# Kernel optimization log

Measured on AMD Instinct MI355X. Metric: run time of the kernel, lower is better.

Reference implementation:

```python
import jax, jax.numpy as jnp
import numpy as np

D_MODEL = 32   # channels arg = Mamba d_model
D_INNER = 32   # expand=1
D_STATE = 8
DT_RANK = 2    # ceil(32/16)
D_CONV = 4


def layer_norm(h, g, b, eps=1e-5):
    m = jnp.mean(h, axis=-1, keepdims=True)
    v = jnp.var(h, axis=-1, keepdims=True)
    return (h - m) * jax.lax.rsqrt(v + eps) * g + b


def causal_conv1d(h, w, b):
    # h: [B, d, L]; w: [d, K] depthwise; torch Conv1d(padding=K-1) truncated to first L
    out = jax.lax.conv_general_dilated(h, w[:, None, :], (1,), [(D_CONV - 1, 0)],
                                       dimension_numbers=('NCH', 'OIH', 'NCH'),
                                       feature_group_count=h.shape[1])
    return out + b[None, :, None]


def selective_scan(u, delta, A, Bm, Cm, D):
    # u, delta: [B, d, L]; A: [d, n]; Bm, Cm: [B, n, L]; D: [d]
    dA = jnp.exp(jnp.einsum('bdl,dn->lbdn', delta, A))       # [L, B, d, n]
    dBu = jnp.einsum('bdl,bnl,bdl->lbdn', delta, Bm, u)      # [L, B, d, n]
    Cseq = jnp.transpose(Cm, (2, 0, 1))                      # [L, B, n]
    h0 = jnp.zeros((u.shape[0], A.shape[0], A.shape[1]), u.dtype)

    def step(h, inp):
        dA_t, dBu_t, C_t = inp
        h = dA_t * h + dBu_t
        return h, jnp.einsum('bdn,bn->bd', h, C_t)

    _, ys = jax.lax.scan(step, h0, (dA, dBu, Cseq))          # ys: [L, B, d]
    return jnp.transpose(ys, (1, 2, 0)) + D[None, :, None] * u


def mamba_direction(xz, conv_w, conv_b, xproj_w, dtproj_w, dtproj_b, A_log, D):
    xh, z = jnp.split(xz, 2, axis=1)                         # each [B, d_inner, L]
    xh = jax.nn.silu(causal_conv1d(xh, conv_w, conv_b))
    x_dbl = jnp.einsum('bdl,kd->bkl', xh, xproj_w)           # [B, dt_rank+2n, L]
    dt, Bm, Cm = jnp.split(x_dbl, [DT_RANK, DT_RANK + D_STATE], axis=1)
    dt = jax.nn.softplus(jnp.einsum('brl,dr->bdl', dt, dtproj_w) + dtproj_b[None, :, None])
    y = selective_scan(xh, dt, -jnp.exp(A_log), Bm, Cm, D)
    return y * jax.nn.silu(z)


def forward(x, lin1_w, lin1_b, ln1_g, ln1_b, in_proj_w,
            conv_w_f, conv_b_f, xproj_w_f, dtproj_w_f, dtproj_b_f, A_log_f, D_f,
            conv_w_r, conv_b_r, xproj_w_r, dtproj_w_r, dtproj_b_r, A_log_r, D_r,
            out_proj_w, mnorm_g, mnorm_b, lin2_w, lin2_b):
    avg = jnp.mean(x, axis=(2, 3))                           # [B, C] adaptive avg pool
    mx = jnp.max(x, axis=(2, 3))                             # [B, C] adaptive max pool
    combined = jnp.stack([avg, mx], axis=-1)                 # [B, C, 2]
    h = combined @ lin1_w.T + lin1_b                         # [B, C, d_model]
    h = layer_norm(h, ln1_g, ln1_b)
    # bidirectional Mamba (bimamba v2) over sequence length L = C
    xz = jnp.einsum('blc,ec->bel', h, in_proj_w)             # [B, 2*d_inner, L]
    out_f = mamba_direction(xz, conv_w_f, conv_b_f, xproj_w_f, dtproj_w_f, dtproj_b_f, A_log_f, D_f)
    out_r = mamba_direction(xz[..., ::-1], conv_w_r, conv_b_r, xproj_w_r, dtproj_w_r, dtproj_b_r, A_log_r, D_r)[..., ::-1]
    out = (out_f + out_r) / 2.0                              # if_devide_out=True
    out = jnp.einsum('bdl,od->blo', out, out_proj_w)         # [B, L, d_model]
    out = layer_norm(out, mnorm_g, mnorm_b)                  # use_norm=True
    att = jax.nn.sigmoid(out @ lin2_w.T + lin2_b)            # [B, L, 1]
    return att[..., None] * 0.25 + 0.875                     # [B, C, 1, 1]


def setup_inputs() -> dict:
    key = jax.random.key(0)
    ks = jax.random.split(key, 12)
    B, C, H, W = 32, 512, 64, 64

    def rn(k, shape, s):
        return jax.random.normal(k, shape, jnp.float32) * s

    A_log = jnp.log(jnp.broadcast_to(jnp.arange(1, D_STATE + 1, dtype=jnp.float32), (D_INNER, D_STATE)))
    return {
        'x': jax.random.normal(ks[0], (B, C, H, W), jnp.float32),
        'lin1_w': rn(ks[1], (D_MODEL, 2), 0.5),
        'lin1_b': jnp.zeros((D_MODEL,), jnp.float32),
        'ln1_g': jnp.ones((D_MODEL,), jnp.float32),
        'ln1_b': jnp.zeros((D_MODEL,), jnp.float32),
        'in_proj_w': rn(ks[2], (2 * D_INNER, D_MODEL), 0.1),
        'conv_w_f': rn(ks[3], (D_INNER, D_CONV), 0.3),
        'conv_b_f': jnp.zeros((D_INNER,), jnp.float32),
        'xproj_w_f': rn(ks[4], (DT_RANK + 2 * D_STATE, D_INNER), 0.1),
        'dtproj_w_f': rn(ks[5], (D_INNER, DT_RANK), 0.5),
        'dtproj_b_f': jnp.full((D_INNER,), -4.6, jnp.float32),
        'A_log_f': A_log,
        'D_f': jnp.ones((D_INNER,), jnp.float32),
        'conv_w_r': rn(ks[6], (D_INNER, D_CONV), 0.3),
        'conv_b_r': jnp.zeros((D_INNER,), jnp.float32),
        'xproj_w_r': rn(ks[7], (DT_RANK + 2 * D_STATE, D_INNER), 0.1),
        'dtproj_w_r': rn(ks[8], (D_INNER, DT_RANK), 0.5),
        'dtproj_b_r': jnp.full((D_INNER,), -4.6, jnp.float32),
        'A_log_r': A_log,
        'D_r': jnp.ones((D_INNER,), jnp.float32),
        'out_proj_w': rn(ks[9], (D_MODEL, D_INNER), 0.1),
        'mnorm_g': jnp.ones((D_MODEL,), jnp.float32),
        'mnorm_b': jnp.zeros((D_MODEL,), jnp.float32),
        'lin2_w': rn(ks[10], (1, D_MODEL), 0.3),
        'lin2_b': jnp.zeros((1,), jnp.float32),
    }


def reference(x, lin1_w, lin1_b, ln1_g, ln1_b, in_proj_w,
              conv_w_f, conv_b_f, xproj_w_f, dtproj_w_f, dtproj_b_f, A_log_f, D_f,
              conv_w_r, conv_b_r, xproj_w_r, dtproj_w_r, dtproj_b_r, A_log_r, D_r,
              out_proj_w, mnorm_g, mnorm_b, lin2_w, lin2_b):
    return forward(x, lin1_w, lin1_b, ln1_g, ln1_b, in_proj_w,
                   conv_w_f, conv_b_f, xproj_w_f, dtproj_w_f, dtproj_b_f, A_log_f, D_f,
                   conv_w_r, conv_b_r, xproj_w_r, dtproj_w_r, dtproj_b_r, A_log_r, D_r,
                   out_proj_w, mnorm_g, mnorm_b, lin2_w, lin2_b)
```

## Files before the change

kernel.cpp:

```cpp
#include <hip/hip_runtime.h>
#include <math.h>

#define BB 32
#define CC 512
#define HW 4096
#define DM 32
#define DI 32
#define DS 8
#define KC 4

#define NCH 16
#define CHL 32

__device__ __forceinline__ float siluf(float x) {
    return x / (1.0f + __expf(-x));
}
__device__ __forceinline__ float softplusf(float x) {
    float ax = fabsf(x);
    return fmaxf(x, 0.0f) + log1pf(__expf(-ax));
}

__global__ __launch_bounds__(256) void poolproj_kernel(
    const float* __restrict__ x,
    const float* __restrict__ lin1_w, const float* __restrict__ lin1_b,
    const float* __restrict__ ln1_g, const float* __restrict__ ln1_b,
    const float* __restrict__ in_proj_w, float* __restrict__ xz)
{
    __shared__ float sWp[64][33];
    int tid = threadIdx.x;
    for (int i = tid; i < 64 * DM; i += 256) sWp[i >> 5][i & 31] = in_proj_w[i];
    __syncthreads();

    int wave = tid >> 6, lane = tid & 63;
    int row = blockIdx.x * 4 + wave;
    const float4* xp = reinterpret_cast<const float4*>(x + (size_t)row * HW);
    float s = 0.f, m = -INFINITY;
#pragma unroll
    for (int k = 0; k < 16; ++k) {
        float4 v = xp[k * 64 + lane];
        s += (v.x + v.y) + (v.z + v.w);
        m = fmaxf(m, fmaxf(fmaxf(v.x, v.y), fmaxf(v.z, v.w)));
    }
#pragma unroll
    for (int off = 1; off < 64; off <<= 1) {
        s += __shfl_xor(s, off);
        m = fmaxf(m, __shfl_xor(m, off));
    }
    float a = s * (1.0f / HW);
    int m_ = lane & 31;
    float h = a * lin1_w[2 * m_] + m * lin1_w[2 * m_ + 1] + lin1_b[m_];
    float sum = h;
#pragma unroll
    for (int mask = 1; mask < 32; mask <<= 1) sum += __shfl_xor(sum, mask);
    float mean = sum * (1.0f / DM);
    float d = h - mean;
    float vs = d * d;
#pragma unroll
    for (int mask = 1; mask < 32; mask <<= 1) vs += __shfl_xor(vs, mask);
    float rs = rsqrtf(vs * (1.0f / DM) + 1e-5f);
    float hn = d * rs * ln1_g[m_] + ln1_b[m_];
    float acc = 0.f;
#pragma unroll
    for (int mm = 0; mm < DM; ++mm)
        acc += __shfl(hn, mm) * sWp[lane][mm];
    xz[((size_t)row << 6) + lane] = acc;
}

__global__ __launch_bounds__(512) void convscan1_kernel(
    const float* __restrict__ xz,
    const float* __restrict__ conv_w_f, const float* __restrict__ conv_b_f,
    const float* __restrict__ xproj_w_f, const float* __restrict__ dtproj_w_f,
    const float* __restrict__ dtproj_b_f,
    const float* __restrict__ conv_w_r, const float* __restrict__ conv_b_r,
    const float* __restrict__ xproj_w_r, const float* __restrict__ dtproj_w_r,
    const float* __restrict__ dtproj_b_r,
    const float* __restrict__ A_log_f, const float* __restrict__ A_log_r,
    float* __restrict__ u_g, float* __restrict__ dt_g,
    float* __restrict__ B_g, float* __restrict__ C_g,
    float* __restrict__ carrA, float* __restrict__ carrH)
{
    int bx = blockIdx.x;
    int b = bx >> 4, t = bx & 15;
    int tid = threadIdx.x;
    int L0 = t * CHL;

    __shared__ float xt[32][41];
    __shared__ float xw_s[2][18][33];
    __shared__ float u_s[2][CHL][33];
    __shared__ float dt_s[2][CHL][33];
    __shared__ float B_s[2][CHL][9];
    __shared__ float C_s[2][CHL][9];
    __shared__ float dtr_s[2][CHL][2];

    for (int idx = tid; idx < 38 * 32; idx += 512) {
        int c = idx >> 5, dd = idx & 31;
        int col = L0 - 3 + c;
        float v = 0.f;
        if (col >= 0 && col < 512)
            v = xz[(((size_t)b * 512 + col) << 6) + dd];
        xt[dd][c] = v;
    }
    for (int idx = tid; idx < 2 * 18 * 32; idx += 512) {
        int dirw = idx >= 576;
        int r2 = idx - dirw * 576;
        const float* xw = dirw ? xproj_w_r : xproj_w_f;
        xw_s[dirw][r2 >> 5][r2 & 31] = xw[r2];
    }
    __syncthreads();

#pragma unroll
    for (int p = 0; p < 4; ++p) {
        int idx = p * 512 + tid;
        int dd = idx & 31, l = (idx >> 5) & 31, dirw = idx >> 10;
        const float* cw2 = dirw ? conv_w_r : conv_w_f;
        const float* cb2 = dirw ? conv_b_r : conv_b_f;
        float acc = cb2[dd];
        if (dirw == 0) {
#pragma unroll
            for (int k = 0; k < KC; ++k) acc += cw2[dd * KC + k] * xt[dd][l + k];
        } else {
#pragma unroll
            for (int jj = 0; jj < KC; ++jj) acc += cw2[dd * KC + 3 - jj] * xt[dd][l + 3 + jj];
        }
        u_s[dirw][l][dd] = siluf(acc);
    }
    __syncthreads();

#pragma unroll
    for (int p = 0; p < 3; ++p) {
        int idx = p * 512 + tid;
        if (idx < 1152) {
            int dirw = idx >= 576;
            int r2 = idx - dirw * 576;
            int o = r2 >> 5, l = r2 & 31;
            float acc = 0.f;
#pragma unroll
            for (int m_ = 0; m_ < 32; ++m_) acc += u_s[dirw][l][m_] * xw_s[dirw][o][m_];
            if (o < 2)       dtr_s[dirw][l][o] = acc;
            else if (o < 10) B_s[dirw][l][o - 2] = acc;
            else             C_s[dirw][l][o - 10] = acc;
        }
    }
    __syncthreads();

#pragma unroll
    for (int p = 0; p < 4; ++p) {
        int idx = p * 512 + tid;
        int dd = idx & 31, l = (idx >> 5) & 31, dirw = idx >> 10;
        const float* dw2 = dirw ? dtproj_w_r : dtproj_w_f;
        const float* db2 = dirw ? dtproj_b_r : dtproj_b_f;
        float v = dtr_s[dirw][l][0] * dw2[dd * 2] + dtr_s[dirw][l][1] * dw2[dd * 2 + 1] + db2[dd];
        dt_s[dirw][l][dd] = softplusf(v);
    }
    __syncthreads();

#pragma unroll
    for (int p = 0; p < 4; ++p) {
        int idx = p * 512 + tid;
        int dd = idx & 31, l = (idx >> 5) & 31, dirw = idx >> 10;
        int sp = dirw ? (511 - (L0 + l)) : (L0 + l);
        size_t g = ((size_t)(b * 2 + dirw) * 512 + sp) * 32 + dd;
        u_g[g]  = u_s[dirw][l][dd];
        dt_g[g] = dt_s[dirw][l][dd];
    }
    {
        int dirw = tid >> 8;
        int r2 = tid & 255;
        int l = r2 >> 3, n = r2 & 7;
        int sp = dirw ? (511 - (L0 + l)) : (L0 + l);
        size_t g = ((size_t)(b * 2 + dirw) * 512 + sp) * 8 + n;
        B_g[g] = B_s[dirw][l][n];
        C_g[g] = C_s[dirw][l][n];
    }

    {
        int dir = tid >> 8;
        int tid2 = tid & 255;
        int dd = tid2 >> 3, nn = tid2 & 7;
        int jc = dir ? (15 - t) : t;
        const float* Alog = dir ? A_log_r : A_log_f;
        float Aa = -__expf(Alog[tid2]);
        float ap = 1.f, h = 0.f;
#pragma unroll 4
        for (int sl = 0; sl < CHL; ++sl) {
            int ll = dir ? (CHL - 1 - sl) : sl;
            float dtv = dt_s[dir][ll][dd];
            float uu  = u_s[dir][ll][dd];
            float bm  = B_s[dir][ll][nn];
            float dA  = __expf(dtv * Aa);
            ap *= dA;
            h = dA * h + dtv * uu * bm;
        }
        size_t cidx = (((size_t)(b * 2 + dir) * NCH + jc) << 8) + tid2;
        carrA[cidx] = ap;
        carrH[cidx] = h;
    }
}

__global__ __launch_bounds__(512) void scan2final_kernel(
    const float* __restrict__ u_g, const float* __restrict__ dt_g,
    const float* __restrict__ B_g, const float* __restrict__ C_g,
    const float* __restrict__ carrA, const float* __restrict__ carrH,
    const float* __restrict__ A_log_f, const float* __restrict__ D_f,
    const float* __restrict__ A_log_r, const float* __restrict__ D_r,
    const float* __restrict__ xz,
    const float* __restrict__ out_proj_w, const float* __restrict__ mnorm_g,
    const float* __restrict__ mnorm_b, const float* __restrict__ lin2_w,
    const float* __restrict__ lin2_b, float* __restrict__ out)
{
    int bx = blockIdx.x;
    int b = bx >> 4, t = bx & 15;
    int tid = threadIdx.x;
    int L0 = t * CHL;

    __shared__ float u_s[2][CHL][33];
    __shared__ float dt_s[2][CHL][33];
    __shared__ float B_s[2][CHL][12];
    __shared__ float C_s[2][CHL][12];
    __shared__ float z_s[CHL][33];
    __shared__ float y_s[2][CHL][33];
    __shared__ float comb_s[CHL][33];
    __shared__ float opw_s[DM][33];

    for (int idx = tid; idx < 2 * CHL * 32; idx += 512) {
        int dirw = idx >> 10;
        int r2 = idx & 1023;
        int sl = r2 >> 5, d = r2 & 31;
        int bd = b * 2 + dirw;
        int tc = dirw ? (15 - t) : t;
        size_t g = ((size_t)bd * 512 + tc * CHL + sl) * 32 + d;
        u_s[dirw][sl][d]  = u_g[g];
        dt_s[dirw][sl][d] = dt_g[g];
    }
    {
        int dirw = tid >> 8;
        int r2 = tid & 255;
        int sl = r2 >> 3, n = r2 & 7;
        int bd = b * 2 + dirw;
        int tc = dirw ? (15 - t) : t;
        size_t g = ((size_t)bd * 512 + tc * CHL + sl) * 8 + n;
        B_s[dirw][sl][n] = B_g[g];
        C_s[dirw][sl][n] = C_g[g];
    }
    for (int idx = tid; idx < CHL * 32; idx += 512) {
        int l = idx >> 5, d = idx & 31;
        z_s[l][d] = xz[(((size_t)b * 512 + L0 + l) << 6) + 32 + d];
        opw_s[idx >> 5][d] = out_proj_w[idx];
    }
    __syncthreads();

    {
        int dir = tid >> 8;
        int r = tid & 255;
        int d = r >> 3, n = r & 7;
        int bd = b * 2 + dir;
        int tt = dir ? (15 - t) : t;
        const float* Alog = dir ? A_log_r : A_log_f;
        const float* Dp   = dir ? D_r : D_f;
        float A  = -__expf(Alog[r]);
        float Dd = Dp[d];

        float h = 0.f;
        for (int g4 = 0; g4 < 4; ++g4) {
            int jbase = g4 * 4;
            if (jbase >= tt) break;
            float av[4], hv[4];
#pragma unroll
            for (int k = 0; k < 4; ++k) {
                int jj = jbase + k;
                int js = (jj < tt) ? jj : 0;
                size_t cb2 = (((size_t)bd * NCH + js) << 8) + r;
                av[k] = carrA[cb2];
                hv[k] = carrH[cb2];
            }
#pragma unroll
            for (int k = 0; k < 4; ++k)
                if (jbase + k < tt) h = av[k] * h + hv[k];
        }

#pragma unroll 4
        for (int sl = 0; sl < CHL; ++sl) {
            float dtv = dt_s[dir][sl][d];
            float uu  = u_s[dir][sl][d];
            float bm  = B_s[dir][sl][n];
            float cm  = C_s[dir][sl][n];
            h = __expf(dtv * A) * h + dtv * uu * bm;
            float py = h * cm;
            py += __shfl_xor(py, 1);
            py += __shfl_xor(py, 2);
            py += __shfl_xor(py, 4);
            if (n == 0) {
                int ll = dir ? (CHL - 1 - sl) : sl;
                y_s[dir][ll][d] = py + Dd * uu;
            }
        }
    }
    __syncthreads();

    for (int idx = tid; idx < CHL * 32; idx += 512) {
        int l = idx >> 5, d = idx & 31;
        comb_s[l][d] = 0.5f * (y_s[0][l][d] + y_s[1][l][d]) * siluf(z_s[l][d]);
    }
    __syncthreads();

    {
        int l = tid >> 4, k = tid & 15;
        float oa = 0.f, ob = 0.f;
#pragma unroll
        for (int d = 0; d < DI; ++d) {
            float c = comb_s[l][d];
            oa += c * opw_s[k][d];
            ob += c * opw_s[k + 16][d];
        }
        float sum = oa + ob;
#pragma unroll
        for (int mask = 1; mask < 16; mask <<= 1) sum += __shfl_xor(sum, mask);
        float mean = sum * (1.0f / DM);
        float da = oa - mean, db2 = ob - mean;
        float vs = da * da + db2 * db2;
#pragma unroll
        for (int mask = 1; mask < 16; mask <<= 1) vs += __shfl_xor(vs, mask);
        float rs = rsqrtf(vs * (1.0f / DM) + 1e-5f);
        float va = da * rs * mnorm_g[k] + mnorm_b[k];
        float vb = db2 * rs * mnorm_g[k + 16] + mnorm_b[k + 16];
        float sv = va * lin2_w[k] + vb * lin2_w[k + 16];
#pragma unroll
        for (int mask = 1; mask < 16; mask <<= 1) sv += __shfl_xor(sv, mask);
        if (k == 0) {
            float att = 1.0f / (1.0f + __expf(-(sv + lin2_b[0])));
            out[(size_t)b * 512 + L0 + l] = 0.25f * att + 0.875f;
        }
    }
}

extern "C" void kernel_launch(void* const* d_in, const int* in_sizes, int n_in,
                              void* d_out, int out_size, void* d_ws, size_t ws_size,
                              hipStream_t stream)
{
    const float* x         = (const float*)d_in[0];
    const float* lin1_w    = (const float*)d_in[1];
    const float* lin1_b    = (const float*)d_in[2];
    const float* ln1_g     = (const float*)d_in[3];
    const float* ln1_b     = (const float*)d_in[4];
    const float* in_proj_w = (const float*)d_in[5];
    const float* conv_w_f  = (const float*)d_in[6];
    const float* conv_b_f  = (const float*)d_in[7];
    const float* xproj_w_f = (const float*)d_in[8];
    const float* dtproj_w_f= (const float*)d_in[9];
    const float* dtproj_b_f= (const float*)d_in[10];
    const float* A_log_f   = (const float*)d_in[11];
    const float* D_f       = (const float*)d_in[12];
    const float* conv_w_r  = (const float*)d_in[13];
    const float* conv_b_r  = (const float*)d_in[14];
    const float* xproj_w_r = (const float*)d_in[15];
    const float* dtproj_w_r= (const float*)d_in[16];
    const float* dtproj_b_r= (const float*)d_in[17];
    const float* A_log_r   = (const float*)d_in[18];
    const float* D_r       = (const float*)d_in[19];
    const float* out_proj_w= (const float*)d_in[20];
    const float* mnorm_g   = (const float*)d_in[21];
    const float* mnorm_b   = (const float*)d_in[22];
    const float* lin2_w    = (const float*)d_in[23];
    const float* lin2_b    = (const float*)d_in[24];

    float* ws   = (float*)d_ws;
    float* xz   = ws;
    float* u_g  = xz + 1048576;
    float* dt_g = u_g + 1048576;
    float* B_g  = dt_g + 1048576;
    float* C_g  = B_g + 262144;
    float* carrA= C_g + 262144;
    float* carrH= carrA + 262144;
    (void)ws_size; (void)in_sizes; (void)n_in; (void)out_size;

    poolproj_kernel<<<4096, 256, 0, stream>>>(x, lin1_w, lin1_b, ln1_g, ln1_b, in_proj_w, xz);
    convscan1_kernel<<<BB * NCH, 512, 0, stream>>>(
        xz, conv_w_f, conv_b_f, xproj_w_f, dtproj_w_f, dtproj_b_f,
        conv_w_r, conv_b_r, xproj_w_r, dtproj_w_r, dtproj_b_r,
        A_log_f, A_log_r, u_g, dt_g, B_g, C_g, carrA, carrH);
    scan2final_kernel<<<BB * NCH, 512, 0, stream>>>(
        u_g, dt_g, B_g, C_g, carrA, carrH,
        A_log_f, D_f, A_log_r, D_r, xz,
        out_proj_w, mnorm_g, mnorm_b, lin2_w, lin2_b, (float*)d_out);
}
```

Baseline: 76.90 us.

## Recompute conv and projections in second scan kernel instead of storing intermediates

The first scan kernel no longer writes u, dt, B and C to global memory and skips computing the C projection. The second kernel reloads xz and recomputes the depthwise conv, x_proj and dt_proj for its chunk in shared memory. This removes the global write and read-back of the intermediate tensors in exchange for duplicated arithmetic and larger shared memory use in the second kernel.

```diff
diff --git a/kernel.cpp b/kernel.cpp
--- a/kernel.cpp
+++ b/kernel.cpp
@@ -75,8 +75,6 @@
     const float* __restrict__ xproj_w_r, const float* __restrict__ dtproj_w_r,
     const float* __restrict__ dtproj_b_r,
     const float* __restrict__ A_log_f, const float* __restrict__ A_log_r,
-    float* __restrict__ u_g, float* __restrict__ dt_g,
-    float* __restrict__ B_g, float* __restrict__ C_g,
     float* __restrict__ carrA, float* __restrict__ carrH)
 {
     int bx = blockIdx.x;
@@ -85,11 +83,10 @@
     int L0 = t * CHL;
 
     __shared__ float xt[32][41];
-    __shared__ float xw_s[2][18][33];
+    __shared__ float xw_s[2][10][33];
     __shared__ float u_s[2][CHL][33];
     __shared__ float dt_s[2][CHL][33];
     __shared__ float B_s[2][CHL][9];
-    __shared__ float C_s[2][CHL][9];
     __shared__ float dtr_s[2][CHL][2];
 
     for (int idx = tid; idx < 38 * 32; idx += 512) {
@@ -100,9 +97,9 @@
             v = xz[(((size_t)b * 512 + col) << 6) + dd];
         xt[dd][c] = v;
     }
-    for (int idx = tid; idx < 2 * 18 * 32; idx += 512) {
-        int dirw = idx >= 576;
-        int r2 = idx - dirw * 576;
+    for (int idx = tid; idx < 2 * 10 * 32; idx += 512) {
+        int dirw = idx >= 320;
+        int r2 = idx - dirw * 320;
         const float* xw = dirw ? xproj_w_r : xproj_w_f;
         xw_s[dirw][r2 >> 5][r2 & 31] = xw[r2];
     }
@@ -127,18 +124,17 @@
     __syncthreads();
 
 #pragma unroll
-    for (int p = 0; p < 3; ++p) {
-        int idx = p * 512 + tid;
-        if (idx < 1152) {
-            int dirw = idx >= 576;
-            int r2 = idx - dirw * 576;
+    for (int p = 0; p < 2; ++p) {
+        int idx = p * 512 + tid;
+        if (idx < 640) {
+            int dirw = idx >= 320;
+            int r2 = idx - dirw * 320;
             int o = r2 >> 5, l = r2 & 31;
             float acc = 0.f;
 #pragma unroll
             for (int m_ = 0; m_ < 32; ++m_) acc += u_s[dirw][l][m_] * xw_s[dirw][o][m_];
-            if (o < 2)       dtr_s[dirw][l][o] = acc;
-            else if (o < 10) B_s[dirw][l][o - 2] = acc;
-            else             C_s[dirw][l][o - 10] = acc;
+            if (o < 2) dtr_s[dirw][l][o] = acc;
+            else       B_s[dirw][l][o - 2] = acc;
         }
     }
     __syncthreads();
@@ -153,25 +149,6 @@
         dt_s[dirw][l][dd] = softplusf(v);
     }
     __syncthreads();
-
-#pragma unroll
-    for (int p = 0; p < 4; ++p) {
-        int idx = p * 512 + tid;
-        int dd = idx & 31, l = (idx >> 5) & 31, dirw = idx >> 10;
-        int sp = dirw ? (511 - (L0 + l)) : (L0 + l);
-        size_t g = ((size_t)(b * 2 + dirw) * 512 + sp) * 32 + dd;
-        u_g[g]  = u_s[dirw][l][dd];
-        dt_g[g] = dt_s[dirw][l][dd];
-    }
-    {
-        int dirw = tid >> 8;
-        int r2 = tid & 255;
-        int l = r2 >> 3, n = r2 & 7;
-        int sp = dirw ? (511 - (L0 + l)) : (L0 + l);
-        size_t g = ((size_t)(b * 2 + dirw) * 512 + sp) * 8 + n;
-        B_g[g] = B_s[dirw][l][n];
-        C_g[g] = C_s[dirw][l][n];
-    }
 
     {
         int dir = tid >> 8;
@@ -198,12 +175,16 @@
 }
 
 __global__ __launch_bounds__(512) void scan2final_kernel(
-    const float* __restrict__ u_g, const float* __restrict__ dt_g,
-    const float* __restrict__ B_g, const float* __restrict__ C_g,
+    const float* __restrict__ xz,
     const float* __restrict__ carrA, const float* __restrict__ carrH,
+    const float* __restrict__ conv_w_f, const float* __restrict__ conv_b_f,
+    const float* __restrict__ xproj_w_f, const float* __restrict__ dtproj_w_f,
+    const float* __restrict__ dtproj_b_f,
+    const float* __restrict__ conv_w_r, const float* __restrict__ conv_b_r,
+    const float* __restrict__ xproj_w_r, const float* __restrict__ dtproj_w_r,
+    const float* __restrict__ dtproj_b_r,
     const float* __restrict__ A_log_f, const float* __restrict__ D_f,
     const float* __restrict__ A_log_r, const float* __restrict__ D_r,
-    const float* __restrict__ xz,
     const float* __restrict__ out_proj_w, const float* __restrict__ mnorm_g,
     const float* __restrict__ mnorm_b, const float* __restrict__ lin2_w,
     const float* __restrict__ lin2_b, float* __restrict__ out)
@@ -213,39 +194,77 @@
     int tid = threadIdx.x;
     int L0 = t * CHL;
 
+    __shared__ float xt[32][41];
+    __shared__ float xw_s[2][18][33];
     __shared__ float u_s[2][CHL][33];
     __shared__ float dt_s[2][CHL][33];
-    __shared__ float B_s[2][CHL][12];
-    __shared__ float C_s[2][CHL][12];
-    __shared__ float z_s[CHL][33];
+    __shared__ float B_s[2][CHL][9];
+    __shared__ float C_s[2][CHL][9];
+    __shared__ float dtr_s[2][CHL][2];
     __shared__ float y_s[2][CHL][33];
     __shared__ float comb_s[CHL][33];
     __shared__ float opw_s[DM][33];
 
-    for (int idx = tid; idx < 2 * CHL * 32; idx += 512) {
-        int dirw = idx >> 10;
-        int r2 = idx & 1023;
-        int sl = r2 >> 5, d = r2 & 31;
-        int bd = b * 2 + dirw;
-        int tc = dirw ? (15 - t) : t;
-        size_t g = ((size_t)bd * 512 + tc * CHL + sl) * 32 + d;
-        u_s[dirw][sl][d]  = u_g[g];
-        dt_s[dirw][sl][d] = dt_g[g];
-    }
-    {
-        int dirw = tid >> 8;
-        int r2 = tid & 255;
-        int sl = r2 >> 3, n = r2 & 7;
-        int bd = b * 2 + dirw;
-        int tc = dirw ? (15 - t) : t;
-        size_t g = ((size_t)bd * 512 + tc * CHL + sl) * 8 + n;
-        B_s[dirw][sl][n] = B_g[g];
-        C_s[dirw][sl][n] = C_g[g];
-    }
-    for (int idx = tid; idx < CHL * 32; idx += 512) {
-        int l = idx >> 5, d = idx & 31;
-        z_s[l][d] = xz[(((size_t)b * 512 + L0 + l) << 6) + 32 + d];
-        opw_s[idx >> 5][d] = out_proj_w[idx];
+    for (int idx = tid; idx < 38 * 32; idx += 512) {
+        int c = idx >> 5, dd = idx & 31;
+        int col = L0 - 3 + c;
+        float v = 0.f;
+        if (col >= 0 && col < 512)
+            v = xz[(((size_t)b * 512 + col) << 6) + dd];
+        xt[dd][c] = v;
+    }
+    for (int idx = tid; idx < 2 * 18 * 32; idx += 512) {
+        int dirw = idx >= 576;
+        int r2 = idx - dirw * 576;
+        const float* xw = dirw ? xproj_w_r : xproj_w_f;
+        xw_s[dirw][r2 >> 5][r2 & 31] = xw[r2];
+    }
+    for (int idx = tid; idx < DM * 32; idx += 512) opw_s[idx >> 5][idx & 31] = out_proj_w[idx];
+    __syncthreads();
+
+#pragma unroll
+    for (int p = 0; p < 4; ++p) {
+        int idx = p * 512 + tid;
+        int dd = idx & 31, l = (idx >> 5) & 31, dirw = idx >> 10;
+        const float* cw2 = dirw ? conv_w_r : conv_w_f;
+        const float* cb2 = dirw ? conv_b_r : conv_b_f;
+        float acc = cb2[dd];
+        if (dirw == 0) {
+#pragma unroll
+            for (int k = 0; k < KC; ++k) acc += cw2[dd * KC + k] * xt[dd][l + k];
+        } else {
+#pragma unroll
+            for (int jj = 0; jj < KC; ++jj) acc += cw2[dd * KC + 3 - jj] * xt[dd][l + 3 + jj];
+        }
+        u_s[dirw][l][dd] = siluf(acc);
+    }
+    __syncthreads();
+
+#pragma unroll
+    for (int p = 0; p < 3; ++p) {
+        int idx = p * 512 + tid;
+        if (idx < 1152) {
+            int dirw = idx >= 576;
+            int r2 = idx - dirw * 576;
+            int o = r2 >> 5, l = r2 & 31;
+            float acc = 0.f;
+#pragma unroll
+            for (int m_ = 0; m_ < 32; ++m_) acc += u_s[dirw][l][m_] * xw_s[dirw][o][m_];
+            if (o < 2)       dtr_s[dirw][l][o] = acc;
+            else if (o < 10) B_s[dirw][l][o - 2] = acc;
+            else             C_s[dirw][l][o - 10] = acc;
+        }
+    }
+    __syncthreads();
+
+#pragma unroll
+    for (int p = 0; p < 4; ++p) {
+        int idx = p * 512 + tid;
+        int dd = idx & 31, l = (idx >> 5) & 31, dirw = idx >> 10;
+        const float* dw2 = dirw ? dtproj_w_r : dtproj_w_f;
+        const float* db2 = dirw ? dtproj_b_r : dtproj_b_f;
+        float v = dtr_s[dirw][l][0] * dw2[dd * 2] + dtr_s[dirw][l][1] * dw2[dd * 2 + 1] + db2[dd];
+        dt_s[dirw][l][dd] = softplusf(v);
     }
     __syncthreads();
 
@@ -280,26 +299,25 @@
 
 #pragma unroll 4
         for (int sl = 0; sl < CHL; ++sl) {
-            float dtv = dt_s[dir][sl][d];
-            float uu  = u_s[dir][sl][d];
-            float bm  = B_s[dir][sl][n];
-            float cm  = C_s[dir][sl][n];
+            int ll = dir ? (CHL - 1 - sl) : sl;
+            float dtv = dt_s[dir][ll][d];
+            float uu  = u_s[dir][ll][d];
+            float bm  = B_s[dir][ll][n];
+            float cm  = C_s[dir][ll][n];
             h = __expf(dtv * A) * h + dtv * uu * bm;
             float py = h * cm;
             py += __shfl_xor(py, 1);
             py += __shfl_xor(py, 2);
             py += __shfl_xor(py, 4);
-            if (n == 0) {
-                int ll = dir ? (CHL - 1 - sl) : sl;
-                y_s[dir][ll][d] = py + Dd * uu;
-            }
+            if (n == 0) y_s[dir][ll][d] = py + Dd * uu;
         }
     }
     __syncthreads();
 
     for (int idx = tid; idx < CHL * 32; idx += 512) {
         int l = idx >> 5, d = idx & 31;
-        comb_s[l][d] = 0.5f * (y_s[0][l][d] + y_s[1][l][d]) * siluf(z_s[l][d]);
+        float z = xz[(((size_t)b * 512 + L0 + l) << 6) + 32 + d];
+        comb_s[l][d] = 0.5f * (y_s[0][l][d] + y_s[1][l][d]) * siluf(z);
     }
     __syncthreads();
 
@@ -365,11 +383,7 @@
 
     float* ws   = (float*)d_ws;
     float* xz   = ws;
-    float* u_g  = xz + 1048576;
-    float* dt_g = u_g + 1048576;
-    float* B_g  = dt_g + 1048576;
-    float* C_g  = B_g + 262144;
-    float* carrA= C_g + 262144;
+    float* carrA= xz + 1048576;
     float* carrH= carrA + 262144;
     (void)ws_size; (void)in_sizes; (void)n_in; (void)out_size;
 
@@ -377,9 +391,11 @@
     convscan1_kernel<<<BB * NCH, 512, 0, stream>>>(
         xz, conv_w_f, conv_b_f, xproj_w_f, dtproj_w_f, dtproj_b_f,
         conv_w_r, conv_b_r, xproj_w_r, dtproj_w_r, dtproj_b_r,
-        A_log_f, A_log_r, u_g, dt_g, B_g, C_g, carrA, carrH);
+        A_log_f, A_log_r, carrA, carrH);
     scan2final_kernel<<<BB * NCH, 512, 0, stream>>>(
-        u_g, dt_g, B_g, C_g, carrA, carrH,
-        A_log_f, D_f, A_log_r, D_r, xz,
+        xz, carrA, carrH,
+        conv_w_f, conv_b_f, xproj_w_f, dtproj_w_f, dtproj_b_f,
+        conv_w_r, conv_b_r, xproj_w_r, dtproj_w_r, dtproj_b_r,
+        A_log_f, D_f, A_log_r, D_r,
         out_proj_w, mnorm_g, mnorm_b, lin2_w, lin2_b, (float*)d_out);
 }
```

After: 79.24 us. 1.03x slower.
